# Kernel tuning notes

Measured on AMD Instinct MI355X. Metric: run time of the kernel, lower is better.

The kernel has to match this reference:

```python
import jax, jax.numpy as jnp
import numpy as np

NGRAMS = (1, 2, 3, 4)


def _conv1d(x, W, b):
    # x: [B, S, E], W: [D, E, K], b: [D] -> [B, S-K+1, D] (valid conv, torch Conv1d)
    y = jax.lax.conv_general_dilated(
        x.transpose(0, 2, 1), W, window_strides=(1,), padding='VALID',
        dimension_numbers=('NCH', 'OIH', 'NCH'))
    return y.transpose(0, 2, 1) + b


def setup_inputs() -> dict:
    key = jax.random.key(0)
    ks = jax.random.split(key, 9)
    B, S, E, D = 64, 512, 256, 512
    inp = {'features': jax.random.normal(ks[0], (B, S, E), dtype=jnp.float32)}
    for i, n in enumerate(NGRAMS):
        fan_in = E * n
        inp[f'W{n}'] = jax.random.normal(ks[1 + 2 * i], (D, E, n), dtype=jnp.float32) / np.sqrt(fan_in)
        inp[f'b{n}'] = jax.random.normal(ks[2 + 2 * i], (D,), dtype=jnp.float32) * 0.01
    return inp


def reference(features, W1, b1, W2, b2, W3, b3, W4, b4):
    Ws = (W1, W2, W3, W4)
    bs = (b1, b2, b3, b4)
    # n-gram conv branches: branch g has kernel size NGRAMS[g] = g+1, length S - g
    feats = [_conv1d(features, W, b) for W, b in zip(Ws, bs)]
    B, S, E = features.shape
    flen = E  # faithful to original: features_len = features.shape[-1] (the embed dim)
    out = feats[0]  # unigram features, [B, S, D]
    i = jnp.arange(flen)
    add = jnp.zeros((B, flen, out.shape[-1]), out.dtype)
    # Original nested loops: out[:, i] += sum_{g=1}^{maxn-1} sum_{p=max(0,i-g+1)}^{min(i+1,L_g)-1} feats[g][:, p]
    # Computed here with per-branch prefix sums (exclusive) -> windowed sums.
    for g in range(1, max(NGRAMS)):
        y = feats[g]                      # [B, L, D], L = S - g
        L = y.shape[1]
        P = jnp.concatenate([jnp.zeros_like(y[:, :1]), jnp.cumsum(y, axis=1)], axis=1)  # [B, L+1, D]
        hi = jnp.minimum(i + 1, L)
        lo = jnp.minimum(jnp.maximum(0, i - g + 1), L)
        win = P[:, hi] - P[:, lo]         # [B, flen, D]
        add = add + jnp.where((hi > lo)[None, :, None], win, jnp.zeros_like(win))
    return out.at[:, :flen].add(add)
```

## Files before the change

kernel.cpp:

```cpp
#include <hip/hip_runtime.h>
#include <hip/hip_bf16.h>

#define EDIM 256
#define SDIM 512
#define BDIM 64
#define DDIM 512
#define SPAD 514

#define OFF_XP    0u
#define OFF_BFI   16842752u
#define OFF_BFT   18415616u
#define OFF_CORR  18677760u
#define OFF_BI    18939904u

#define CVT_BLOCKS  4112
#define BF_BASE     4112
#define CORR_BASE   4560
#define PREP_BLOCKS 8656

typedef __attribute__((ext_vector_type(8))) __bf16 bf16x8;
typedef __attribute__((ext_vector_type(4))) float  f32x4;
typedef __attribute__((ext_vector_type(8))) unsigned short ushort8v;

__device__ __forceinline__ unsigned short f2bf(float f) {
    unsigned int u = __float_as_uint(f);
    u = (u + 0x7fffu + ((u >> 16) & 1u)) >> 16;
    return (unsigned short)u;
}

__global__ __launch_bounds__(256) void prep_all(
    const float* __restrict__ X,
    const float* __restrict__ W1, const float* __restrict__ b1,
    const float* __restrict__ W2, const float* __restrict__ b2,
    const float* __restrict__ W3, const float* __restrict__ b3,
    const float* __restrict__ W4, const float* __restrict__ b4,
    char* __restrict__ wsb)
{
    const int tid = threadIdx.x;

    if (blockIdx.x < CVT_BLOCKS) {
        unsigned short* Xp = (unsigned short*)(wsb + OFF_XP);
        const int i   = blockIdx.x * 256 + tid;
        const int row = i >> 5;
        const int q   = i & 31;
        const int b   = row / SPAD;
        const int j   = row - b * SPAD;
        ushort8v v;
        if (j < 2) {
            v = (ushort8v)0;
        } else {
            const float* src = X + ((size_t)(b * SDIM + j - 2)) * EDIM + q * 8;
            const float4 f0 = *(const float4*)(src);
            const float4 f1 = *(const float4*)(src + 4);
            v[0] = f2bf(f0.x); v[1] = f2bf(f0.y); v[2] = f2bf(f0.z); v[3] = f2bf(f0.w);
            v[4] = f2bf(f1.x); v[5] = f2bf(f1.y); v[6] = f2bf(f1.z); v[7] = f2bf(f1.w);
        }
        *(ushort8v*)(Xp + (size_t)row * EDIM + q * 8) = v;
        return;
    }

    if (blockIdx.x < CORR_BASE) {
        const int p  = blockIdx.x - BF_BASE;
        const int t  = tid >> 6;
        const int l  = tid & 63;
        const int fm = l & 15;
        const int hi = l >> 4;
        if (p < 384) {
            const int kt = p % 48;
            const int h  = (p / 48) & 1;
            const int c  = p / 96;
            const int d  = c * 128 + h * 64 + t * 16 + fm;
            const int shift = kt >> 3;
            const int e0 = (kt & 7) * 32 + hi * 8;
            ushort8v v;
#pragma unroll
            for (int j = 0; j < 8; ++j) {
                const int e  = e0 + j;
                const int de = d * 256 + e;
                float g;
                if      (shift == 0) g = W4[de*4+0];
                else if (shift == 1) g = W3[de*3+0] + W4[de*4+0] + W4[de*4+1];
                else if (shift == 2) g = W1[de] + W2[de*2+0] + W3[de*3+0] + W3[de*3+1]
                                       + W4[de*4+0] + W4[de*4+1] + W4[de*4+2];
                else if (shift == 3) g = W2[de*2+1] + W3[de*3+1] + W3[de*3+2]
                                       + W4[de*4+1] + W4[de*4+2] + W4[de*4+3];
                else if (shift == 4) g = W3[de*3+2] + W4[de*4+2] + W4[de*4+3];
                else                 g = W4[de*4+3];
                v[j] = f2bf(g);
            }
            *(ushort8v*)(wsb + OFF_BFI + (size_t)((((c*2+h)*48 + kt)*4 + t)*1024 + l*16)) = v;
            if (kt == 0 && hi == 0)
                ((float*)(wsb + OFF_BI))[d] = b1[d] + b2[d] + 2.0f*b3[d] + 3.0f*b4[d];
        } else {
            const int q  = p - 384;
            const int kt = q % 8;
            const int h  = (q / 8) & 1;
            const int c  = q / 16;
            const int d  = c * 128 + h * 64 + t * 16 + fm;
            const int k0 = kt * 32 + hi * 8;
            ushort8v v;
#pragma unroll
            for (int j = 0; j < 8; ++j) v[j] = f2bf(W1[d * 256 + k0 + j]);
            *(ushort8v*)(wsb + OFF_BFT + (size_t)((((c*2+h)*8 + kt)*4 + t)*1024 + l*16)) = v;
        }
        return;
    }

    {
        __shared__ float cls[16];
        const int cb = blockIdx.x - CORR_BASE;
        const int d  = cb >> 3;
        const int bq = (cb & 7) * 8;
        const int e  = tid;

        if (tid < 16) cls[tid] = 0.f;

        const float w31 = W3[(size_t)d * 768 + 3 * e + 1];
        const float w32 = W3[(size_t)d * 768 + 3 * e + 2];
        const float4 w4v = *(const float4*)(W4 + (size_t)d * 1024 + 4 * e);
        const float w41 = w4v.y, w42 = w4v.z, w43 = w4v.w;

        const float c00 = w31 + w41 + w42;
        const float c01 = w32 + w42 + w43;
        const float c02 = w43;
        __syncthreads();

#pragma unroll
        for (int bi = 0; bi < 8; ++bi) {
            const float* xr = X + (size_t)(bq + bi) * (SDIM * EDIM) + e;
            const float x0 = xr[0], x1 = xr[EDIM], x2 = xr[2 * EDIM];
            float a0 = c00 * x0 + c01 * x1 + c02 * x2;
            float a1 = w41 * x0 + w42 * x1 + w43 * x2;
#pragma unroll
            for (int off = 32; off >= 1; off >>= 1) {
                a0 += __shfl_xor(a0, off, 64);
                a1 += __shfl_xor(a1, off, 64);
            }
            if ((tid & 63) == 0) {
                atomicAdd(&cls[bi * 2 + 0], a0);
                atomicAdd(&cls[bi * 2 + 1], a1);
            }
        }
        __syncthreads();

        if (tid < 16) {
            const int s = tid & 1;
            const float bc = s ? b4[d] : (b3[d] + 2.f * b4[d]);
            ((float*)(wsb + OFF_CORR))[(size_t)d * 128 + bq * 2 + tid] = -cls[tid] - bc;
        }
    }
}

#define GLL(src, dst) \
    __builtin_amdgcn_global_load_lds((const __attribute__((address_space(1))) void*)(src), \
                                     (__attribute__((address_space(3))) void*)(dst), 16, 0, 0)

__global__ __launch_bounds__(256) void mega(
    const unsigned short* __restrict__ Xp,
    const char* __restrict__ wsb,
    const float* __restrict__ b1,
    float* __restrict__ out)
{
    __shared__ __align__(16) char smem[16384];
    const int id  = blockIdx.x;
    const int strip = id & 127;
    const int c     = id >> 7;
    const int col0  = c * 128;
    const int tid = threadIdx.x;
    const int w = tid >> 6, l = tid & 63;

    const int sub = l >> 2;
    const int swz = (((l & 3) ^ ((sub >> 1) & 3)) * 16);
    const int ra0 = strip * 128 + 32 * w + sub;
    const int ra1 = ra0 + 16;
    const int ba0 = ra0 >> 8, sa0 = ra0 & 255;
    const int ba1 = ra1 >> 8, sa1 = ra1 & 255;

    const int oA0 = (32 * w) * 64;
    const int oA1 = (32 * w + 16) * 64;
    char* pc = smem;
    char* pn = smem + 8192;

    const int wr = (w >> 1) * 64;
    const int h  = w & 1;
    const int wc = h * 64;
    const int fm = l & 15;
    const int rslot = (((l >> 4) ^ ((fm >> 1) & 3)) * 16);

    const char* bfi = wsb + OFF_BFI + (size_t)(c * 2 + h) * (48 * 4096) + l * 16;
    const char* bft = wsb + OFF_BFT + (size_t)(c * 2 + h) * (8 * 4096) + l * 16;

    f32x4 acc[4][4];
    const char *a0, *a1;

    auto LOADB = [&](bf16x8 (&dst)[4], const char* base, int kt) {
#pragma unroll
        for (int t = 0; t < 4; ++t)
            dst[t] = *(const bf16x8*)(base + (size_t)kt * 4096 + t * 1024);
    };
    auto STAGE = [&](char* buf) {
        GLL(a0, buf + oA0);
        GLL(a1, buf + oA1);
        a0 += 64; a1 += 64;
    };
    auto COMP = [&](const char* buf, const bf16x8 (&bfr)[4]) {
        bf16x8 af[4];
#pragma unroll
        for (int t = 0; t < 4; ++t)
            af[t] = *(const bf16x8*)(buf + (wr + t * 16 + fm) * 64 + rslot);
#pragma unroll
        for (int i = 0; i < 4; ++i)
#pragma unroll
            for (int j = 0; j < 4; ++j)
                acc[i][j] = __builtin_amdgcn_mfma_f32_16x16x32_bf16(af[i], bfr[j], acc[i][j], 0, 0, 0);
    };

    auto GEMM = [&](const char* bbase, int nk) {
        bf16x8 bA[4], bB[4];
        LOADB(bA, bbase, 0);
        STAGE(pc);
#pragma unroll 1
        for (int kt = 0; kt < nk; kt += 2) {
            STAGE(pn);
            LOADB(bB, bbase, kt + 1);
            asm volatile("s_waitcnt vmcnt(6)" ::: "memory");
            __builtin_amdgcn_s_barrier();
            __builtin_amdgcn_s_setprio(1);
            COMP(pc, bA);
            __builtin_amdgcn_s_setprio(0);
            asm volatile("s_waitcnt lgkmcnt(0)" ::: "memory");
            __builtin_amdgcn_s_barrier();
            if (kt + 2 < nk) {
                STAGE(pc);
                LOADB(bA, bbase, kt + 2);
                asm volatile("s_waitcnt vmcnt(6)" ::: "memory");
            } else {
                asm volatile("s_waitcnt vmcnt(0)" ::: "memory");
            }
            __builtin_amdgcn_s_barrier();
            __builtin_amdgcn_s_setprio(1);
            COMP(pn, bB);
            __builtin_amdgcn_s_setprio(0);
            asm volatile("s_waitcnt lgkmcnt(0)" ::: "memory");
            __builtin_amdgcn_s_barrier();
        }
    };

    auto EPI = [&](int s_base, bool with_corr) {
        const float* bias = with_corr ? (const float*)(wsb + OFF_BI) : b1;
        const float* corr = (const float*)(wsb + OFF_CORR);
        const int ocol = col0 + wc + fm;
        const int rq   = (l >> 4) * 4;
        float bv[4];
#pragma unroll
        for (int j = 0; j < 4; ++j) bv[j] = bias[ocol + j * 16];
#pragma unroll
        for (int i = 0; i < 4; ++i) {
#pragma unroll
            for (int r = 0; r < 4; ++r) {
                const int rr  = strip * 128 + wr + i * 16 + rq + r;
                const int ssl = rr & 255;
                const int bb  = rr >> 8;
                float* op = out + ((size_t)(bb * SDIM + s_base + ssl)) * DDIM + ocol;
                if (with_corr && ssl < 2) {
                    const float* cp = corr + (size_t)ocol * 128 + bb * 2 + ssl;
#pragma unroll
                    for (int j = 0; j < 4; ++j)
                        op[j * 16] = acc[i][j][r] + bv[j] + cp[(size_t)j * 16 * 128];
                } else {
#pragma unroll
                    for (int j = 0; j < 4; ++j)
                        op[j * 16] = acc[i][j][r] + bv[j];
                }
            }
        }
    };

#pragma unroll
    for (int i = 0; i < 4; ++i)
#pragma unroll
        for (int j = 0; j < 4; ++j) acc[i][j] = (f32x4){0.f, 0.f, 0.f, 0.f};
    a0 = (const char*)(Xp + (size_t)(ba0 * SPAD + sa0) * EDIM) + swz;
    a1 = (const char*)(Xp + (size_t)(ba1 * SPAD + sa1) * EDIM) + swz;
    GEMM(bfi, 48);
    EPI(0, true);

#pragma unroll
    for (int i = 0; i < 4; ++i)
#pragma unroll
        for (int j = 0; j < 4; ++j) acc[i][j] = (f32x4){0.f, 0.f, 0.f, 0.f};
    a0 = (const char*)(Xp + (size_t)(ba0 * SPAD + 258 + sa0) * EDIM) + swz;
    a1 = (const char*)(Xp + (size_t)(ba1 * SPAD + 258 + sa1) * EDIM) + swz;
    GEMM(bft, 8);
    EPI(256, false);
}

extern "C" void kernel_launch(void* const* d_in, const int* in_sizes, int n_in,
                              void* d_out, int out_size, void* d_ws, size_t ws_size,
                              hipStream_t stream)
{
    const float* X  = (const float*)d_in[0];
    const float* W1 = (const float*)d_in[1];
    const float* b1 = (const float*)d_in[2];
    const float* W2 = (const float*)d_in[3];
    const float* b2 = (const float*)d_in[4];
    const float* W3 = (const float*)d_in[5];
    const float* b3 = (const float*)d_in[6];
    const float* W4 = (const float*)d_in[7];
    const float* b4 = (const float*)d_in[8];
    float* out = (float*)d_out;
    char*  wsb = (char*)d_ws;

    prep_all<<<dim3(PREP_BLOCKS), dim3(256), 0, stream>>>(X, W1, b1, W2, b2, W3, b3, W4, b4, wsb);

    mega<<<dim3(512), dim3(256), 0, stream>>>(
        (const unsigned short*)(wsb + OFF_XP), wsb, b1, out);
}
```

Measured before the change: 163.3 us.

## Deepen GEMM pipeline to four LDS stages and restructure weight prep

The main GEMM loop moves from a two-buffer to a four-buffer LDS ring, issuing loads two k-steps ahead with one barrier per phase instead of two. The goal is to hide global-load latency better and cut synchronisation overhead. LDS use doubles to 32 KB and launch bounds now request 2 blocks per SM. Weight prep is also rewritten so each block handles one output channel with coalesced weight reads and scattered 2-byte stores, instead of strided gathers.

```diff
diff --git a/kernel.cpp b/kernel.cpp
--- a/kernel.cpp
+++ b/kernel.cpp
@@ -14,9 +14,9 @@
 #define OFF_BI    18939904u
 
 #define CVT_BLOCKS  4112
-#define BF_BASE     4112
-#define CORR_BASE   4560
-#define PREP_BLOCKS 8656
+#define WB_BASE     4112
+#define CORR_BASE   4624
+#define PREP_BLOCKS 8720
 
 typedef __attribute__((ext_vector_type(8))) __bf16 bf16x8;
 typedef __attribute__((ext_vector_type(4))) float  f32x4;
@@ -60,49 +60,36 @@
     }
 
     if (blockIdx.x < CORR_BASE) {
-        const int p  = blockIdx.x - BF_BASE;
-        const int t  = tid >> 6;
-        const int l  = tid & 63;
-        const int fm = l & 15;
-        const int hi = l >> 4;
-        if (p < 384) {
-            const int kt = p % 48;
-            const int h  = (p / 48) & 1;
-            const int c  = p / 96;
-            const int d  = c * 128 + h * 64 + t * 16 + fm;
-            const int shift = kt >> 3;
-            const int e0 = (kt & 7) * 32 + hi * 8;
-            ushort8v v;
-#pragma unroll
-            for (int j = 0; j < 8; ++j) {
-                const int e  = e0 + j;
-                const int de = d * 256 + e;
-                float g;
-                if      (shift == 0) g = W4[de*4+0];
-                else if (shift == 1) g = W3[de*3+0] + W4[de*4+0] + W4[de*4+1];
-                else if (shift == 2) g = W1[de] + W2[de*2+0] + W3[de*3+0] + W3[de*3+1]
-                                       + W4[de*4+0] + W4[de*4+1] + W4[de*4+2];
-                else if (shift == 3) g = W2[de*2+1] + W3[de*3+1] + W3[de*3+2]
-                                       + W4[de*4+1] + W4[de*4+2] + W4[de*4+3];
-                else if (shift == 4) g = W3[de*3+2] + W4[de*4+2] + W4[de*4+3];
-                else                 g = W4[de*4+3];
-                v[j] = f2bf(g);
-            }
-            *(ushort8v*)(wsb + OFF_BFI + (size_t)((((c*2+h)*48 + kt)*4 + t)*1024 + l*16)) = v;
-            if (kt == 0 && hi == 0)
-                ((float*)(wsb + OFF_BI))[d] = b1[d] + b2[d] + 2.0f*b3[d] + 3.0f*b4[d];
-        } else {
-            const int q  = p - 384;
-            const int kt = q % 8;
-            const int h  = (q / 8) & 1;
-            const int c  = q / 16;
-            const int d  = c * 128 + h * 64 + t * 16 + fm;
-            const int k0 = kt * 32 + hi * 8;
-            ushort8v v;
-#pragma unroll
-            for (int j = 0; j < 8; ++j) v[j] = f2bf(W1[d * 256 + k0 + j]);
-            *(ushort8v*)(wsb + OFF_BFT + (size_t)((((c*2+h)*8 + kt)*4 + t)*1024 + l*16)) = v;
-        }
+        const int d = blockIdx.x - WB_BASE;
+        const int e = tid;
+        const int de = d * EDIM + e;
+
+        const float w1  = W1[de];
+        const float w20 = W2[de * 2 + 0], w21 = W2[de * 2 + 1];
+        const float w30 = W3[de * 3 + 0], w31 = W3[de * 3 + 1], w32 = W3[de * 3 + 2];
+        const float w40 = W4[de * 4 + 0], w41 = W4[de * 4 + 1], w42 = W4[de * 4 + 2], w43 = W4[de * 4 + 3];
+
+        float g[6];
+        g[0] = w40;
+        g[1] = w30 + w40 + w41;
+        g[2] = w1 + w20 + w30 + w31 + w40 + w41 + w42;
+        g[3] = w21 + w31 + w32 + w41 + w42 + w43;
+        g[4] = w32 + w42 + w43;
+        g[5] = w43;
+
+        const int fm = d & 15, t = (d >> 4) & 3, h = (d >> 6) & 1, c = d >> 7;
+        const int hi = (e >> 3) & 3, j = e & 7, eb = e >> 5;
+        char* ibase = wsb + OFF_BFI + (size_t)((c * 2 + h) * 48) * 4096
+                    + t * 1024 + hi * 256 + fm * 16 + j * 2;
+#pragma unroll
+        for (int s = 0; s < 6; ++s)
+            *(unsigned short*)(ibase + (size_t)(s * 8 + eb) * 4096) = f2bf(g[s]);
+
+        *(unsigned short*)(wsb + OFF_BFT + (size_t)((c * 2 + h) * 8 + eb) * 4096
+                           + t * 1024 + hi * 256 + fm * 16 + j * 2) = f2bf(w1);
+
+        if (e == 0)
+            ((float*)(wsb + OFF_BI))[d] = b1[d] + b2[d] + 2.0f * b3[d] + 3.0f * b4[d];
         return;
     }
 
@@ -155,13 +142,13 @@
     __builtin_amdgcn_global_load_lds((const __attribute__((address_space(1))) void*)(src), \
                                      (__attribute__((address_space(3))) void*)(dst), 16, 0, 0)
 
-__global__ __launch_bounds__(256) void mega(
+__global__ __launch_bounds__(256, 2) void mega(
     const unsigned short* __restrict__ Xp,
     const char* __restrict__ wsb,
     const float* __restrict__ b1,
     float* __restrict__ out)
 {
-    __shared__ __align__(16) char smem[16384];
+    __shared__ __align__(16) char smem[32768];
     const int id  = blockIdx.x;
     const int strip = id & 127;
     const int c     = id >> 7;
@@ -178,8 +165,10 @@
 
     const int oA0 = (32 * w) * 64;
     const int oA1 = (32 * w + 16) * 64;
-    char* pc = smem;
-    char* pn = smem + 8192;
+    char* q0 = smem;
+    char* q1 = smem + 8192;
+    char* q2 = smem + 16384;
+    char* q3 = smem + 24576;
 
     const int wr = (w >> 1) * 64;
     const int h  = w & 1;
@@ -215,35 +204,27 @@
                 acc[i][j] = __builtin_amdgcn_mfma_f32_16x16x32_bf16(af[i], bfr[j], acc[i][j], 0, 0, 0);
     };
 
+#define PHASE_W6  asm volatile("s_waitcnt vmcnt(6) lgkmcnt(0)" ::: "memory"); \
+                  __builtin_amdgcn_s_barrier();
+#define PHASE_W0  asm volatile("s_waitcnt vmcnt(0) lgkmcnt(0)" ::: "memory"); \
+                  __builtin_amdgcn_s_barrier();
+#define DO_COMP(Q, B) __builtin_amdgcn_s_setprio(1); COMP(Q, B); __builtin_amdgcn_s_setprio(0);
+
     auto GEMM = [&](const char* bbase, int nk) {
-        bf16x8 bA[4], bB[4];
-        LOADB(bA, bbase, 0);
-        STAGE(pc);
+        bf16x8 b0[4], b1r[4], b2[4], b3[4];
+        STAGE(q0); LOADB(b0,  bbase, 0);
+        STAGE(q1); LOADB(b1r, bbase, 1);
 #pragma unroll 1
-        for (int kt = 0; kt < nk; kt += 2) {
-            STAGE(pn);
-            LOADB(bB, bbase, kt + 1);
-            asm volatile("s_waitcnt vmcnt(6)" ::: "memory");
-            __builtin_amdgcn_s_barrier();
-            __builtin_amdgcn_s_setprio(1);
-            COMP(pc, bA);
-            __builtin_amdgcn_s_setprio(0);
-            asm volatile("s_waitcnt lgkmcnt(0)" ::: "memory");
-            __builtin_amdgcn_s_barrier();
-            if (kt + 2 < nk) {
-                STAGE(pc);
-                LOADB(bA, bbase, kt + 2);
-                asm volatile("s_waitcnt vmcnt(6)" ::: "memory");
-            } else {
-                asm volatile("s_waitcnt vmcnt(0)" ::: "memory");
-            }
-            __builtin_amdgcn_s_barrier();
-            __builtin_amdgcn_s_setprio(1);
-            COMP(pn, bB);
-            __builtin_amdgcn_s_setprio(0);
-            asm volatile("s_waitcnt lgkmcnt(0)" ::: "memory");
-            __builtin_amdgcn_s_barrier();
-        }
+        for (int kt = 0; kt + 4 < nk; kt += 4) {
+            PHASE_W6; STAGE(q2); LOADB(b2,  bbase, kt + 2); DO_COMP(q0, b0);
+            PHASE_W6; STAGE(q3); LOADB(b3,  bbase, kt + 3); DO_COMP(q1, b1r);
+            PHASE_W6; STAGE(q0); LOADB(b0,  bbase, kt + 4); DO_COMP(q2, b2);
+            PHASE_W6; STAGE(q1); LOADB(b1r, bbase, kt + 5); DO_COMP(q3, b3);
+        }
+        PHASE_W6; STAGE(q2); LOADB(b2, bbase, nk - 2); DO_COMP(q0, b0);
+        PHASE_W6; STAGE(q3); LOADB(b3, bbase, nk - 1); DO_COMP(q1, b1r);
+        PHASE_W6;                                      DO_COMP(q2, b2);
+        PHASE_W0;                                      DO_COMP(q3, b3);
     };
 
     auto EPI = [&](int s_base, bool with_corr) {
```

Measured after the change: 160.3 us. Within noise of the previous version (-1.9%).
